# Optimization experiments

Hardware: AMD Instinct MI355X
Metric: run time of the kernel (lower is better)

The kernel has to match this reference:

```python
import jax, jax.numpy as jnp
import numpy as np

# Model dims: N = polynomial degree, RANK = CP rank, HxW image, S = flattened size
N, RANK, H, W = 4, 128, 256, 256
S = H * W
B = 32
EPS = 1e-5  # torch BatchNorm2d default eps


def setup_inputs() -> dict:
    key = jax.random.key(0)
    ks = jax.random.split(key, 4)
    x = jax.random.normal(ks[0], (B, 1, H, W), dtype=jnp.float32)
    # PolyLayer (PolyGAN CCP) parameters: per-degree factors U_n [S, RANK],
    # output projection C [S, RANK], output bias beta [S]
    U = jax.random.normal(ks[1], (N, S, RANK), dtype=jnp.float32) * 0.02
    C = jax.random.normal(ks[2], (S, RANK), dtype=jnp.float32) * 0.02
    beta = jax.random.normal(ks[3], (S,), dtype=jnp.float32) * 0.02
    # BatchNorm2d(1) affine params (torch default init: weight=1, bias=0)
    gamma = jnp.ones((1,), dtype=jnp.float32)
    bn_bias = jnp.zeros((1,), dtype=jnp.float32)
    return {"x": x, "U": U, "C": C, "beta": beta, "gamma": gamma, "bn_bias": bn_bias}


def reference(x, U, C, beta, gamma, bn_bias):
    b = x.shape[0]
    # BatchNorm2d(num_features=1), training mode: biased batch stats over (N,H,W)
    mean = jnp.mean(x, axis=(0, 2, 3), keepdims=True)
    var = jnp.var(x, axis=(0, 2, 3), keepdims=True)
    xn = (x - mean) * jax.lax.rsqrt(var + EPS)
    xn = xn * gamma.reshape(1, -1, 1, 1) + bn_bias.reshape(1, -1, 1, 1)
    # Flatten each sample: [B, S]. The torch Generator applies PolyLayer
    # per-sample across Python threads; here it is one batched call.
    z = xn.reshape(b, S)
    # CCP polynomial: t_n = U_n^T z for each degree -> [N, B, RANK]
    t = jnp.einsum('bs,nsr->nbr', z, U)
    h = t[0]
    for n in range(1, N):  # fixed small degree loop (structural, not data dim)
        h = t[n] * h + h   # h_n = (U_n^T z) * h_{n-1} + h_{n-1}
    out = h @ C.T + beta   # project back to image space: [B, S]
    return out.reshape(b, 1, H, W)
```

## Files before the change

kernel.cpp:

```cpp
#include <hip/hip_runtime.h>

#define SDIM 65536
#define BDIM 32
#define RDIM 128
#define NDEG 4
#define NCHUNK 256
#define CHUNK_S (SDIM / NCHUNK)
#define MTOT (BDIM * SDIM)
#define EPS_BN 1e-5f
#define NSTATB 512

__global__ void k_stats(const float* __restrict__ x, float* __restrict__ partial) {
    __shared__ float s_sum[256];
    __shared__ float s_sq[256];
    int tid = threadIdx.x;
    int gid = blockIdx.x * 256 + tid;
    int stride = gridDim.x * 256;
    float sum = 0.f, sq = 0.f;
    const float4* x4 = (const float4*)x;
    for (int i = gid; i < MTOT / 4; i += stride) {
        float4 v = x4[i];
        sum += (v.x + v.y) + (v.z + v.w);
        sq  += (v.x * v.x + v.y * v.y) + (v.z * v.z + v.w * v.w);
    }
    s_sum[tid] = sum; s_sq[tid] = sq;
    __syncthreads();
    for (int off = 128; off > 0; off >>= 1) {
        if (tid < off) { s_sum[tid] += s_sum[tid + off]; s_sq[tid] += s_sq[tid + off]; }
        __syncthreads();
    }
    if (tid == 0) { partial[blockIdx.x * 2] = s_sum[0]; partial[blockIdx.x * 2 + 1] = s_sq[0]; }
}

__global__ void k_stats_fin(const float* __restrict__ partial, float* __restrict__ stats) {
    __shared__ float s_sum[256];
    __shared__ float s_sq[256];
    int tid = threadIdx.x;
    float sum = partial[tid * 2] + partial[(tid + 256) * 2];
    float sq  = partial[tid * 2 + 1] + partial[(tid + 256) * 2 + 1];
    s_sum[tid] = sum; s_sq[tid] = sq;
    __syncthreads();
    for (int off = 128; off > 0; off >>= 1) {
        if (tid < off) { s_sum[tid] += s_sum[tid + off]; s_sq[tid] += s_sq[tid + off]; }
        __syncthreads();
    }
    if (tid == 0) { stats[0] = s_sum[0]; stats[1] = s_sq[0]; }
}

__global__ void __launch_bounds__(256) k_norm_t(const float* __restrict__ x,
                                                const float* __restrict__ gamma,
                                                const float* __restrict__ bnb,
                                                const float* __restrict__ stats,
                                                float* __restrict__ zT) {
    __shared__ float lds[64][33];
    int tid = threadIdx.x;
    int s0 = blockIdx.x * 64;
    float mean = stats[0] * (1.f / MTOT);
    float var  = stats[1] * (1.f / MTOT) - mean * mean;
    float istd = rsqrtf(var + EPS_BN);
    float a  = gamma[0] * istd;
    float c0 = bnb[0] - mean * a;

    int sl = tid & 63, bq = tid >> 6;
#pragma unroll
    for (int k = 0; k < 8; ++k) {
        int b = k * 4 + bq;
        lds[sl][b] = fmaf(a, x[(size_t)b * SDIM + s0 + sl], c0);
    }
    __syncthreads();
    int bl = tid & 31, sq = tid >> 5;
#pragma unroll
    for (int k = 0; k < 8; ++k) {
        int s = k * 8 + sq;
        zT[(size_t)(s0 + s) * BDIM + bl] = lds[s][bl];
    }
}

__global__ void __launch_bounds__(256) k_gemm_t(const float* __restrict__ zT,
                                                const float* __restrict__ U,
                                                float* __restrict__ t_part) {
    __shared__ float lds[2 * BDIM * RDIM];
    int tid  = threadIdx.x;
    int r    = tid & 127;
    int half = __builtin_amdgcn_readfirstlane(tid >> 7);
    int chunk = blockIdx.x;
    int n     = blockIdx.y;
    int s0 = chunk * CHUNK_S + half * (CHUNK_S / 2);

    const float* Ub = U + (size_t)n * SDIM * RDIM;
    float acc[BDIM];
#pragma unroll
    for (int b = 0; b < BDIM; ++b) acc[b] = 0.f;

#pragma unroll 2
    for (int s = s0; s < s0 + CHUNK_S / 2; ++s) {
        float u = Ub[(size_t)s * RDIM + r];
        const float* zr = zT + (size_t)s * BDIM;
#pragma unroll
        for (int b = 0; b < BDIM; ++b)
            acc[b] = fmaf(zr[b], u, acc[b]);
    }

#pragma unroll
    for (int b = 0; b < BDIM; ++b)
        lds[half * (BDIM * RDIM) + b * RDIM + r] = acc[b];
    __syncthreads();

    float* outp = t_part + (size_t)(n * NCHUNK + chunk) * (BDIM * RDIM);
    for (int i = tid; i < BDIM * RDIM; i += 256)
        outp[i] = lds[i] + lds[BDIM * RDIM + i];
}

__global__ void __launch_bounds__(256) k_reduce_h(const float* __restrict__ t_part,
                                                  float* __restrict__ h) {
    __shared__ float lds[NDEG][8][32];
    int tid = threadIdx.x;
    int il = tid & 31;
    int cg = tid >> 5;
    int i0 = blockIdx.x * 32;

#pragma unroll
    for (int n = 0; n < NDEG; ++n) {
        float s = 0.f;
#pragma unroll 4
        for (int k = 0; k < 32; ++k) {
            int c = cg * 32 + k;
            s += t_part[(size_t)(n * NCHUNK + c) * (BDIM * RDIM) + i0 + il];
        }
        lds[n][cg][il] = s;
    }
    __syncthreads();
    if (tid < 32) {
        float t[NDEG];
#pragma unroll
        for (int n = 0; n < NDEG; ++n) {
            float s = 0.f;
#pragma unroll
            for (int g = 0; g < 8; ++g) s += lds[n][g][il];
            t[n] = s;
        }
        float hh = t[0];
#pragma unroll
        for (int n = 1; n < NDEG; ++n) hh = fmaf(t[n], hh, hh);
        h[i0 + il] = hh;
    }
}

__global__ void __launch_bounds__(256) k_out(const float* __restrict__ h,
                                             const float* __restrict__ Cm,
                                             const float* __restrict__ beta,
                                             float* __restrict__ out) {
    int tid = threadIdx.x;
    int s   = (blockIdx.x >> 1) * 64 + (tid & 63);
    int bg  = __builtin_amdgcn_readfirstlane((blockIdx.x & 1) * 4 + (tid >> 6));
    int b0  = bg * 4;

    float acc[4] = {0.f, 0.f, 0.f, 0.f};
    const float4* Cr = (const float4*)(Cm + (size_t)s * RDIM);
    const float* hb = h + b0 * RDIM;

#pragma unroll 8
    for (int rc = 0; rc < RDIM / 4; ++rc) {
        float4 c = Cr[rc];
#pragma unroll
        for (int j = 0; j < 4; ++j) {
            const float* hr = hb + j * RDIM + rc * 4;
            float a = acc[j];
            a = fmaf(c.x, hr[0], a);
            a = fmaf(c.y, hr[1], a);
            a = fmaf(c.z, hr[2], a);
            a = fmaf(c.w, hr[3], a);
            acc[j] = a;
        }
    }
    float bt = beta[s];
#pragma unroll
    for (int j = 0; j < 4; ++j)
        out[(size_t)(b0 + j) * SDIM + s] = acc[j] + bt;
}

extern "C" void kernel_launch(void* const* d_in, const int* in_sizes, int n_in,
                              void* d_out, int out_size, void* d_ws, size_t ws_size,
                              hipStream_t stream) {
    const float* x     = (const float*)d_in[0];
    const float* U     = (const float*)d_in[1];
    const float* Cm    = (const float*)d_in[2];
    const float* beta  = (const float*)d_in[3];
    const float* gamma = (const float*)d_in[4];
    const float* bnb   = (const float*)d_in[5];
    float* out = (float*)d_out;

    char* ws = (char*)d_ws;
    size_t off = 0;
    float* stats   = (float*)(ws + off); off += 256;
    float* partial = (float*)(ws + off); off += NSTATB * 2 * 4;
    float* zT      = (float*)(ws + off); off += (size_t)BDIM * SDIM * 4;
    float* t_part  = (float*)(ws + off); off += (size_t)NDEG * NCHUNK * BDIM * RDIM * 4;
    float* h       = (float*)(ws + off); off += (size_t)BDIM * RDIM * 4;

    k_stats<<<NSTATB, 256, 0, stream>>>(x, partial);
    k_stats_fin<<<1, 256, 0, stream>>>(partial, stats);
    k_norm_t<<<SDIM / 64, 256, 0, stream>>>(x, gamma, bnb, stats, zT);
    dim3 g3(NCHUNK, NDEG);
    k_gemm_t<<<g3, 256, 0, stream>>>(zT, U, t_part);
    k_reduce_h<<<128, 256, 0, stream>>>(t_part, h);
    k_out<<<2048, 256, 0, stream>>>(h, Cm, beta, out);
}
```

Before: 99.26 us.

## Stage z chunk in LDS and retile GEMM threads over batch and rank

```diff
diff --git a/kernel.cpp b/kernel.cpp
--- a/kernel.cpp
+++ b/kernel.cpp
@@ -79,36 +79,51 @@
 __global__ void __launch_bounds__(256) k_gemm_t(const float* __restrict__ zT,
                                                 const float* __restrict__ U,
                                                 float* __restrict__ t_part) {
-    __shared__ float lds[2 * BDIM * RDIM];
+    __shared__ float lds_z[CHUNK_S * BDIM];
     int tid  = threadIdx.x;
-    int r    = tid & 127;
-    int half = __builtin_amdgcn_readfirstlane(tid >> 7);
+    int p    = tid & 63;
+    int o    = __builtin_amdgcn_readfirstlane(tid >> 6);
     int chunk = blockIdx.x;
     int n     = blockIdx.y;
-    int s0 = chunk * CHUNK_S + half * (CHUNK_S / 2);
-
-    const float* Ub = U + (size_t)n * SDIM * RDIM;
-    float acc[BDIM];
-#pragma unroll
-    for (int b = 0; b < BDIM; ++b) acc[b] = 0.f;
+    int s0 = chunk * CHUNK_S;
+
+    {
+        const float4* src4 = (const float4*)(zT + (size_t)s0 * BDIM);
+        float4* dst4 = (float4*)lds_z;
+#pragma unroll
+        for (int i = 0; i < (CHUNK_S * BDIM / 4) / 256; ++i)
+            dst4[i * 256 + tid] = src4[i * 256 + tid];
+    }
+    __syncthreads();
+
+    const float* Ub = U + (size_t)n * SDIM * RDIM + (size_t)s0 * RDIM;
+    const float4* zq = (const float4*)lds_z;
+
+    float acc[8][2];
+#pragma unroll
+    for (int j = 0; j < 8; ++j) { acc[j][0] = 0.f; acc[j][1] = 0.f; }
 
 #pragma unroll 2
-    for (int s = s0; s < s0 + CHUNK_S / 2; ++s) {
-        float u = Ub[(size_t)s * RDIM + r];
-        const float* zr = zT + (size_t)s * BDIM;
-#pragma unroll
-        for (int b = 0; b < BDIM; ++b)
-            acc[b] = fmaf(zr[b], u, acc[b]);
-    }
-
-#pragma unroll
-    for (int b = 0; b < BDIM; ++b)
-        lds[half * (BDIM * RDIM) + b * RDIM + r] = acc[b];
-    __syncthreads();
-
-    float* outp = t_part + (size_t)(n * NCHUNK + chunk) * (BDIM * RDIM);
-    for (int i = tid; i < BDIM * RDIM; i += 256)
-        outp[i] = lds[i] + lds[BDIM * RDIM + i];
+    for (int s = 0; s < CHUNK_S; ++s) {
+        float4 z0 = zq[s * (BDIM / 4) + o * 2];
+        float4 z1 = zq[s * (BDIM / 4) + o * 2 + 1];
+        float2 u2 = *(const float2*)(Ub + (size_t)s * RDIM + 2 * p);
+        acc[0][0] = fmaf(z0.x, u2.x, acc[0][0]); acc[0][1] = fmaf(z0.x, u2.y, acc[0][1]);
+        acc[1][0] = fmaf(z0.y, u2.x, acc[1][0]); acc[1][1] = fmaf(z0.y, u2.y, acc[1][1]);
+        acc[2][0] = fmaf(z0.z, u2.x, acc[2][0]); acc[2][1] = fmaf(z0.z, u2.y, acc[2][1]);
+        acc[3][0] = fmaf(z0.w, u2.x, acc[3][0]); acc[3][1] = fmaf(z0.w, u2.y, acc[3][1]);
+        acc[4][0] = fmaf(z1.x, u2.x, acc[4][0]); acc[4][1] = fmaf(z1.x, u2.y, acc[4][1]);
+        acc[5][0] = fmaf(z1.y, u2.x, acc[5][0]); acc[5][1] = fmaf(z1.y, u2.y, acc[5][1]);
+        acc[6][0] = fmaf(z1.z, u2.x, acc[6][0]); acc[6][1] = fmaf(z1.z, u2.y, acc[6][1]);
+        acc[7][0] = fmaf(z1.w, u2.x, acc[7][0]); acc[7][1] = fmaf(z1.w, u2.y, acc[7][1]);
+    }
+
+    float* outp = t_part + ((size_t)n * NCHUNK + chunk) * (BDIM * RDIM);
+#pragma unroll
+    for (int j = 0; j < 8; ++j) {
+        int b = o * 8 + j;
+        *(float2*)(outp + b * RDIM + 2 * p) = make_float2(acc[j][0], acc[j][1]);
+    }
 }
 
 __global__ void __launch_bounds__(256) k_reduce_h(const float* __restrict__ t_part,
```

New measurement: 111.7 us. +12.5%, slower.

## Register-tile the U^T z GEMM with LDS-staged z and a two-stage split-K reduction

Applied to the files above, without the earlier changes.

```diff
diff --git a/kernel.cpp b/kernel.cpp
--- a/kernel.cpp
+++ b/kernel.cpp
@@ -4,11 +4,13 @@
 #define BDIM 32
 #define RDIM 128
 #define NDEG 4
-#define NCHUNK 256
-#define CHUNK_S (SDIM / NCHUNK)
+#define NCHUNK 512
+#define CHUNK_S 128
 #define MTOT (BDIM * SDIM)
 #define EPS_BN 1e-5f
 #define NSTATB 512
+#define TSLICE (NDEG * BDIM * RDIM)
+#define NGRP 32
 
 __global__ void k_stats(const float* __restrict__ x, float* __restrict__ partial) {
     __shared__ float s_sum[256];
@@ -79,71 +81,139 @@
 __global__ void __launch_bounds__(256) k_gemm_t(const float* __restrict__ zT,
                                                 const float* __restrict__ U,
                                                 float* __restrict__ t_part) {
-    __shared__ float lds[2 * BDIM * RDIM];
-    int tid  = threadIdx.x;
-    int r    = tid & 127;
-    int half = __builtin_amdgcn_readfirstlane(tid >> 7);
+    __shared__ float z_lds[CHUNK_S * BDIM];
+    int tid = threadIdx.x;
+    int pl  = tid >> 6;
+    int ln  = tid & 63;
+    int o   = ln >> 4;
+    int q   = ln & 15;
     int chunk = blockIdx.x;
     int n     = blockIdx.y;
-    int s0 = chunk * CHUNK_S + half * (CHUNK_S / 2);
-
-    const float* Ub = U + (size_t)n * SDIM * RDIM;
-    float acc[BDIM];
-#pragma unroll
-    for (int b = 0; b < BDIM; ++b) acc[b] = 0.f;
+    size_t s0 = (size_t)chunk * CHUNK_S;
+
+    {
+        const float4* src = (const float4*)(zT + s0 * BDIM);
+        float4* dst = (float4*)z_lds;
+#pragma unroll
+        for (int i = 0; i < 4; ++i)
+            dst[i * 256 + tid] = src[i * 256 + tid];
+    }
+    __syncthreads();
+
+    float acc[8][8];
+#pragma unroll
+    for (int j = 0; j < 8; ++j)
+#pragma unroll
+        for (int k = 0; k < 8; ++k) acc[j][k] = 0.f;
+
+    const float* zrow = z_lds + (size_t)pl * 32 * BDIM + 8 * o;
+    const float* urow = U + (size_t)n * SDIM * RDIM + (s0 + pl * 32) * RDIM + 4 * q;
 
 #pragma unroll 2
-    for (int s = s0; s < s0 + CHUNK_S / 2; ++s) {
-        float u = Ub[(size_t)s * RDIM + r];
-        const float* zr = zT + (size_t)s * BDIM;
-#pragma unroll
-        for (int b = 0; b < BDIM; ++b)
-            acc[b] = fmaf(zr[b], u, acc[b]);
-    }
-
-#pragma unroll
-    for (int b = 0; b < BDIM; ++b)
-        lds[half * (BDIM * RDIM) + b * RDIM + r] = acc[b];
-    __syncthreads();
-
-    float* outp = t_part + (size_t)(n * NCHUNK + chunk) * (BDIM * RDIM);
-    for (int i = tid; i < BDIM * RDIM; i += 256)
-        outp[i] = lds[i] + lds[BDIM * RDIM + i];
-}
-
-__global__ void __launch_bounds__(256) k_reduce_h(const float* __restrict__ t_part,
+    for (int rr = 0; rr < 32; ++rr) {
+        float4 za = *(const float4*)(zrow);
+        float4 zb = *(const float4*)(zrow + 4);
+        float4 ua = *(const float4*)(urow);
+        float4 ub = *(const float4*)(urow + 64);
+        float zv[8] = {za.x, za.y, za.z, za.w, zb.x, zb.y, zb.z, zb.w};
+#pragma unroll
+        for (int j = 0; j < 8; ++j) {
+            acc[j][0] = fmaf(zv[j], ua.x, acc[j][0]);
+            acc[j][1] = fmaf(zv[j], ua.y, acc[j][1]);
+            acc[j][2] = fmaf(zv[j], ua.z, acc[j][2]);
+            acc[j][3] = fmaf(zv[j], ua.w, acc[j][3]);
+            acc[j][4] = fmaf(zv[j], ub.x, acc[j][4]);
+            acc[j][5] = fmaf(zv[j], ub.y, acc[j][5]);
+            acc[j][6] = fmaf(zv[j], ub.z, acc[j][6]);
+            acc[j][7] = fmaf(zv[j], ub.w, acc[j][7]);
+        }
+        zrow += BDIM;
+        urow += RDIM;
+    }
+
+    float* cm = z_lds;
+    __syncthreads();
+    if (pl == 1) {
+#pragma unroll
+        for (int j = 0; j < 8; ++j)
+#pragma unroll
+            for (int k = 0; k < 8; ++k) cm[(j * 8 + k) * 64 + ln] = acc[j][k];
+    }
+    __syncthreads();
+    if (pl == 0) {
+#pragma unroll
+        for (int j = 0; j < 8; ++j)
+#pragma unroll
+            for (int k = 0; k < 8; ++k) acc[j][k] += cm[(j * 8 + k) * 64 + ln];
+    }
+    __syncthreads();
+    if (pl == 2) {
+#pragma unroll
+        for (int j = 0; j < 8; ++j)
+#pragma unroll
+            for (int k = 0; k < 8; ++k) cm[(j * 8 + k) * 64 + ln] = acc[j][k];
+    }
+    __syncthreads();
+    if (pl == 0) {
+#pragma unroll
+        for (int j = 0; j < 8; ++j)
+#pragma unroll
+            for (int k = 0; k < 8; ++k) acc[j][k] += cm[(j * 8 + k) * 64 + ln];
+    }
+    __syncthreads();
+    if (pl == 3) {
+#pragma unroll
+        for (int j = 0; j < 8; ++j)
+#pragma unroll
+            for (int k = 0; k < 8; ++k) cm[(j * 8 + k) * 64 + ln] = acc[j][k];
+    }
+    __syncthreads();
+    if (pl == 0) {
+        float* outp = t_part + ((size_t)chunk * NDEG + n) * (BDIM * RDIM);
+#pragma unroll
+        for (int j = 0; j < 8; ++j) {
+#pragma unroll
+            for (int k = 0; k < 8; ++k) acc[j][k] += cm[(j * 8 + k) * 64 + ln];
+            int b = o * 8 + j;
+            *(float4*)(outp + b * RDIM + 4 * q) =
+                make_float4(acc[j][0], acc[j][1], acc[j][2], acc[j][3]);
+            *(float4*)(outp + b * RDIM + 64 + 4 * q) =
+                make_float4(acc[j][4], acc[j][5], acc[j][6], acc[j][7]);
+        }
+    }
+}
+
+__global__ void __launch_bounds__(256) k_reduce_a(const float* __restrict__ t_part,
+                                                  float* __restrict__ t_mid) {
+    int tid = threadIdx.x;
+    int strip = blockIdx.x;
+    int g     = blockIdx.y;
+    int idx4 = strip * 256 + tid;
+    const float4* tp4 = (const float4*)t_part;
+    float4 s = make_float4(0.f, 0.f, 0.f, 0.f);
+#pragma unroll
+    for (int c = 0; c < 16; ++c) {
+        float4 v = tp4[(size_t)(g * 16 + c) * (TSLICE / 4) + idx4];
+        s.x += v.x; s.y += v.y; s.z += v.z; s.w += v.w;
+    }
+    ((float4*)t_mid)[(size_t)g * (TSLICE / 4) + idx4] = s;
+}
+
+__global__ void __launch_bounds__(256) k_reduce_b(const float* __restrict__ t_mid,
                                                   float* __restrict__ h) {
-    __shared__ float lds[NDEG][8][32];
-    int tid = threadIdx.x;
-    int il = tid & 31;
-    int cg = tid >> 5;
-    int i0 = blockIdx.x * 32;
-
-#pragma unroll
-    for (int n = 0; n < NDEG; ++n) {
-        float s = 0.f;
-#pragma unroll 4
-        for (int k = 0; k < 32; ++k) {
-            int c = cg * 32 + k;
-            s += t_part[(size_t)(n * NCHUNK + c) * (BDIM * RDIM) + i0 + il];
-        }
-        lds[n][cg][il] = s;
-    }
-    __syncthreads();
-    if (tid < 32) {
-        float t[NDEG];
-#pragma unroll
-        for (int n = 0; n < NDEG; ++n) {
-            float s = 0.f;
-#pragma unroll
-            for (int g = 0; g < 8; ++g) s += lds[n][g][il];
-            t[n] = s;
-        }
-        float hh = t[0];
-#pragma unroll
-        for (int n = 1; n < NDEG; ++n) hh = fmaf(t[n], hh, hh);
-        h[i0 + il] = hh;
-    }
+    int i = blockIdx.x * 256 + threadIdx.x;
+    float t[NDEG];
+#pragma unroll
+    for (int n = 0; n < NDEG; ++n) t[n] = 0.f;
+    for (int g = 0; g < NGRP; ++g) {
+#pragma unroll
+        for (int n = 0; n < NDEG; ++n)
+            t[n] += t_mid[(size_t)g * TSLICE + n * (BDIM * RDIM) + i];
+    }
+    float hh = t[0];
+#pragma unroll
+    for (int n = 1; n < NDEG; ++n) hh = fmaf(t[n], hh, hh);
+    h[i] = hh;
 }
 
 __global__ void __launch_bounds__(256) k_out(const float* __restrict__ h,
@@ -195,7 +265,8 @@
     float* stats   = (float*)(ws + off); off += 256;
     float* partial = (float*)(ws + off); off += NSTATB * 2 * 4;
     float* zT      = (float*)(ws + off); off += (size_t)BDIM * SDIM * 4;
-    float* t_part  = (float*)(ws + off); off += (size_t)NDEG * NCHUNK * BDIM * RDIM * 4;
+    float* t_part  = (float*)(ws + off); off += (size_t)NCHUNK * TSLICE * 4;
+    float* t_mid   = (float*)(ws + off); off += (size_t)NGRP * TSLICE * 4;
     float* h       = (float*)(ws + off); off += (size_t)BDIM * RDIM * 4;
 
     k_stats<<<NSTATB, 256, 0, stream>>>(x, partial);
@@ -203,6 +274,8 @@
     k_norm_t<<<SDIM / 64, 256, 0, stream>>>(x, gamma, bnb, stats, zT);
     dim3 g3(NCHUNK, NDEG);
     k_gemm_t<<<g3, 256, 0, stream>>>(zT, U, t_part);
-    k_reduce_h<<<128, 256, 0, stream>>>(t_part, h);
+    dim3 g4(16, NGRP);
+    k_reduce_a<<<g4, 256, 0, stream>>>(t_part, t_mid);
+    k_reduce_b<<<16, 256, 0, stream>>>(t_mid, h);
     k_out<<<2048, 256, 0, stream>>>(h, Cm, beta, out);
 }
```

Result: slower. 132.8 us (+33.8%).
